# Optimization experiments

Hardware: AMD Instinct MI355X
Metric: run time of the kernel (lower is better)

## Reference

```python
import jax, jax.numpy as jnp
import numpy as np

T = 2048
HID = 5120
NH = 16
D_NOPE = 128
D_ROPE = 64
D_V = 128
Q_LORA = 1536
KV_LORA = 512
THETA = 10000.0
EPS = 1e-6
QK_HD = D_NOPE + D_ROPE
SCALE = QK_HD ** -0.5


def setup_inputs() -> dict:
    key = jax.random.key(0)
    ks = jax.random.split(key, 8)
    s = 0.02  # weight init scale for numerical stability
    return {
        "positions": jnp.arange(T, dtype=jnp.int32),
        "hidden_states": jax.random.normal(ks[0], (T, HID), jnp.float32),
        "w_qa": jax.random.normal(ks[1], (HID, Q_LORA), jnp.float32) * s,
        "qa_ln_w": jnp.ones((Q_LORA,), jnp.float32),
        "w_qb": jax.random.normal(ks[2], (Q_LORA, NH * QK_HD), jnp.float32) * s,
        "w_kva": jax.random.normal(ks[3], (HID, KV_LORA + D_ROPE), jnp.float32) * s,
        "kva_ln_w": jnp.ones((KV_LORA,), jnp.float32),
        "w_kvb": jax.random.normal(ks[4], (KV_LORA, NH * (D_NOPE + D_V)), jnp.float32) * s,
        "w_o": jax.random.normal(ks[5], (NH * D_V, HID), jnp.float32) * s,
    }


def rmsnorm(x, w):
    var = jnp.mean(x * x, axis=-1, keepdims=True)
    return x * jax.lax.rsqrt(var + EPS) * w


def apply_rope(positions, x):
    # GPT-J (interleaved) style rope on last dim of size D_ROPE; x: [T, H, D_ROPE]
    inv_freq = 1.0 / (THETA ** (jnp.arange(0, D_ROPE, 2, dtype=jnp.float32) / D_ROPE))
    ang = positions.astype(jnp.float32)[:, None] * inv_freq  # [T, D_ROPE/2]
    cos = jnp.cos(ang)[:, None, :]  # [T, 1, D/2]
    sin = jnp.sin(ang)[:, None, :]
    x1 = x[..., 0::2]
    x2 = x[..., 1::2]
    o1 = x1 * cos - x2 * sin
    o2 = x2 * cos + x1 * sin
    return jnp.stack([o1, o2], axis=-1).reshape(x.shape)


def reference(positions, hidden_states, w_qa, qa_ln_w, w_qb, w_kva, kva_ln_w, w_kvb, w_o):
    # --- low-rank Q path ---
    q_c = rmsnorm(hidden_states @ w_qa, qa_ln_w)             # [T, Q_LORA]
    q = (q_c @ w_qb).reshape(T, NH, QK_HD)                   # [T, H, 192]
    q_nope, q_pe = q[..., :D_NOPE], q[..., D_NOPE:]

    # --- compressed KV path ---
    kv = hidden_states @ w_kva                               # [T, KV_LORA + D_ROPE]
    kv_c = rmsnorm(kv[:, :KV_LORA], kva_ln_w)                # [T, 512]
    k_pe = kv[:, KV_LORA:][:, None, :]                       # [T, 1, 64]

    # partial rope
    q_pe = apply_rope(positions, q_pe)                       # [T, H, 64]
    k_pe = apply_rope(positions, k_pe)                       # [T, 1, 64]

    # decompress K_nope / V
    kv_up = (kv_c @ w_kvb).reshape(T, NH, D_NOPE + D_V)
    k_nope, v = kv_up[..., :D_NOPE], kv_up[..., D_NOPE:]     # [T, H, 128] each

    k_pe_b = jnp.broadcast_to(k_pe, (T, NH, D_ROPE))
    q_full = jnp.concatenate([q_nope, q_pe], axis=-1)        # [T, H, 192]
    k_full = jnp.concatenate([k_nope, k_pe_b], axis=-1)      # [T, H, 192]

    # causal attention
    scores = jnp.einsum("thd,shd->hts", q_full, k_full) * SCALE  # [H, T, T]
    causal = positions[:, None] >= positions[None, :]
    scores = jnp.where(causal[None], scores, jnp.finfo(scores.dtype).min)
    probs = jax.nn.softmax(scores, axis=-1)
    attn = jnp.einsum("hts,shd->thd", probs, v)              # [T, H, 128]

    out = attn.reshape(T, NH * D_V) @ w_o                    # [T, HID]
    return out
```

## Files before the change

kernel.cpp:

```cpp
#include <hip/hip_runtime.h>
#include <hip/hip_bf16.h>
#include <math.h>

#define T 2048
#define HID 5120
#define NH 16
#define D_NOPE 128
#define D_ROPE 64
#define D_V 128
#define Q_LORA 1536
#define KV_LORA 512
#define QK_HD 192
#define KVA_N 576
#define KVA_NP 640
#define N_QB (NH*QK_HD)
#define N_KVB (NH*(D_NOPE+D_V))
#define ATT_SCALE 0.07216878364870322f

typedef __bf16 bf16x8_t __attribute__((ext_vector_type(8)));
typedef float f32x4_t __attribute__((ext_vector_type(4)));
typedef unsigned short u16x4 __attribute__((ext_vector_type(4)));
typedef unsigned int u32x4 __attribute__((ext_vector_type(4)));

union BF8 { u16x4 h[2]; unsigned short u[8]; bf16x8_t v; u32x4 q; };

static __device__ __forceinline__ unsigned short f2bf(float f){
  union { float f; unsigned u; } x; x.f = f;
  unsigned r = x.u + 0x7FFFu + ((x.u >> 16) & 1u);
  return (unsigned short)(r >> 16);
}

static __device__ __forceinline__ void gload_lds16(const void* g, void* l){
  __builtin_amdgcn_global_load_lds(
      (const __attribute__((address_space(1))) void*)(unsigned long long)g,
      (__attribute__((address_space(3))) void*)(unsigned int)(unsigned long long)l,
      16, 0, 0);
}

__global__ __launch_bounds__(256) void k_cvt(const float* __restrict__ in,
                                             unsigned short* __restrict__ out, int n4){
  int i = blockIdx.x*256 + threadIdx.x;
  int stride = gridDim.x*256;
  for (; i < n4; i += stride){
    f32x4_t v = ((const f32x4_t*)in)[i];
    u16x4 o; o.x=f2bf(v.x); o.y=f2bf(v.y); o.z=f2bf(v.z); o.w=f2bf(v.w);
    ((u16x4*)out)[i] = o;
  }
}

__global__ __launch_bounds__(256) void k_cvtT(const float* __restrict__ W,
                                              unsigned short* __restrict__ Wt, int K, int N){
  __shared__ float tile[32][33];
  int n0 = blockIdx.x*32, k0 = blockIdx.y*32;
  int r = threadIdx.x >> 3, c4 = (threadIdx.x & 7) * 4;
  f32x4_t v = {0.f,0.f,0.f,0.f};
  if (n0 + c4 < N) v = *(const f32x4_t*)(W + (size_t)(k0 + r)*N + n0 + c4);
  tile[r][c4+0]=v.x; tile[r][c4+1]=v.y; tile[r][c4+2]=v.z; tile[r][c4+3]=v.w;
  __syncthreads();
  u16x4 o;
  o.x = f2bf(tile[c4+0][r]); o.y = f2bf(tile[c4+1][r]);
  o.z = f2bf(tile[c4+2][r]); o.w = f2bf(tile[c4+3][r]);
  *(u16x4*)(Wt + (size_t)(n0 + r)*K + k0 + c4) = o;
}

__global__ __launch_bounds__(256) void k_gemm(const unsigned short* __restrict__ A,
                                              const unsigned short* __restrict__ Bt,
                                              float* __restrict__ C, int M, int N, int K){
  __shared__ unsigned short sA[128*32];
  __shared__ unsigned short sB[128*32];
  int bn = blockIdx.x*128, bm = blockIdx.y*128;
  int tid = threadIdx.x;
  int l = tid & 63, lr = l & 15, lg = l >> 4;
  int w = tid >> 6;
  int wm = (w >> 1)*64, wn = (w & 1)*64;
  f32x4_t acc[4][4];
  f32x4_t z4 = {0.f,0.f,0.f,0.f};
  #pragma unroll
  for (int i=0;i<4;i++)
    #pragma unroll
    for(int j=0;j<4;j++) acc[i][j] = z4;
  for (int k0 = 0; k0 < K; k0 += 32){
    __syncthreads();
    #pragma unroll
    for (int it = 0; it < 2; ++it){
      int c = it*256 + tid;
      int row = c >> 2, kc = (c & 3) * 8;
      gload_lds16(A  + (size_t)(bm + row)*K + k0 + kc, &sA[c*8]);
      gload_lds16(Bt + (size_t)(bn + row)*K + k0 + kc, &sB[c*8]);
    }
    __syncthreads();
    BF8 af[4], bf[4];
    #pragma unroll
    for (int mf=0; mf<4; ++mf)
      af[mf].q = *(const u32x4*)&sA[(wm + mf*16 + lr)*32 + 8*lg];
    #pragma unroll
    for (int nf=0; nf<4; ++nf)
      bf[nf].q = *(const u32x4*)&sB[(wn + nf*16 + lr)*32 + 8*lg];
    #pragma unroll
    for (int mf=0; mf<4; ++mf)
      #pragma unroll
      for (int nf=0; nf<4; ++nf)
        acc[mf][nf] = __builtin_amdgcn_mfma_f32_16x16x32_bf16(af[mf].v, bf[nf].v, acc[mf][nf], 0,0,0);
  }
  #pragma unroll
  for (int mf=0; mf<4; ++mf){
    int row = bm + wm + mf*16 + 4*lg;
    #pragma unroll
    for (int nf=0; nf<4; ++nf){
      int col = bn + wn + nf*16 + lr;
      #pragma unroll
      for (int rg=0; rg<4; ++rg)
        C[(size_t)(row + rg)*N + col] = acc[mf][nf][rg];
    }
  }
}

__global__ __launch_bounds__(256) void k_rms_q(const float* __restrict__ qa,
                                               const float* __restrict__ w,
                                               unsigned short* __restrict__ qc){
  int t = blockIdx.x, tid = threadIdx.x;
  const float* row = qa + (size_t)t*Q_LORA;
  float ss = 0.f;
  for (int i = tid; i < Q_LORA; i += 256){ float x = row[i]; ss += x*x; }
  #pragma unroll
  for (int off=1; off<64; off<<=1) ss += __shfl_xor(ss, off, 64);
  __shared__ float red[4];
  if ((tid & 63) == 0) red[tid>>6] = ss;
  __syncthreads();
  ss = red[0]+red[1]+red[2]+red[3];
  float sc = rsqrtf(ss/(float)Q_LORA + 1e-6f);
  unsigned short* orow = qc + (size_t)t*Q_LORA;
  for (int i = tid; i < Q_LORA; i += 256) orow[i] = f2bf(row[i]*sc*w[i]);
}

__global__ __launch_bounds__(256) void k_rms_kv(const float* __restrict__ kvf,
                                                const float* __restrict__ w,
                                                const int* __restrict__ pos,
                                                unsigned short* __restrict__ kvc,
                                                unsigned short* __restrict__ k_full){
  int t = blockIdx.x, tid = threadIdx.x;
  const float* row = kvf + (size_t)t*KVA_NP;
  float ss = 0.f;
  for (int i = tid; i < KV_LORA; i += 256){ float x = row[i]; ss += x*x; }
  #pragma unroll
  for (int off=1; off<64; off<<=1) ss += __shfl_xor(ss, off, 64);
  __shared__ float red[4];
  if ((tid & 63) == 0) red[tid>>6] = ss;
  __syncthreads();
  ss = red[0]+red[1]+red[2]+red[3];
  float sc = rsqrtf(ss/(float)KV_LORA + 1e-6f);
  for (int i = tid; i < KV_LORA; i += 256)
    kvc[(size_t)t*KV_LORA + i] = f2bf(row[i]*sc*w[i]);
  if (tid < 32){
    int i = tid;
    float x1 = row[KV_LORA + 2*i], x2 = row[KV_LORA + 2*i + 1];
    float p = (float)pos[t];
    float invf = 1.0f / powf(10000.0f, (float)(2*i)/64.0f);
    float sn, cs; sincosf(p*invf, &sn, &cs);
    unsigned short b1 = f2bf(x1*cs - x2*sn), b2 = f2bf(x2*cs + x1*sn);
    for (int h=0; h<NH; ++h){
      unsigned short* kr = k_full + ((size_t)(h*T + t))*QK_HD + D_NOPE + 2*i;
      kr[0] = b1; kr[1] = b2;
    }
  }
}

__global__ __launch_bounds__(256) void k_scat_q(const float* __restrict__ qf,
                                                const int* __restrict__ pos,
                                                unsigned short* __restrict__ q_full){
  int t = blockIdx.x, tid = threadIdx.x;
  const float* row = qf + (size_t)t*N_QB;
  for (int idx = tid; idx < NH*D_NOPE; idx += 256){
    int h = idx >> 7, d = idx & 127;
    q_full[((size_t)(h*T + t))*QK_HD + d] = f2bf(row[h*QK_HD + d] * ATT_SCALE);
  }
  float p = (float)pos[t];
  for (int idx = tid; idx < NH*32; idx += 256){
    int h = idx >> 5, i = idx & 31;
    float x1 = row[h*QK_HD + D_NOPE + 2*i], x2 = row[h*QK_HD + D_NOPE + 2*i+1];
    float invf = 1.0f / powf(10000.0f, (float)(2*i)/64.0f);
    float sn, cs; sincosf(p*invf, &sn, &cs);
    unsigned short* qr = q_full + ((size_t)(h*T + t))*QK_HD + D_NOPE + 2*i;
    qr[0] = f2bf((x1*cs - x2*sn)*ATT_SCALE);
    qr[1] = f2bf((x2*cs + x1*sn)*ATT_SCALE);
  }
}

__global__ __launch_bounds__(256) void k_scat_kv(const float* __restrict__ kvup,
                                                 unsigned short* __restrict__ k_full,
                                                 unsigned short* __restrict__ vt){
  int h = blockIdx.y, t0 = blockIdx.x*32;
  int tid = threadIdx.x;
  __shared__ float vtile[32][129];
  #pragma unroll
  for (int it=0; it<16; ++it){
    int idx = tid + it*256;
    int r = idx >> 7, d = idx & 127;
    float kn = kvup[(size_t)(t0 + r)*N_KVB + h*256 + d];
    k_full[((size_t)(h*T + t0 + r))*QK_HD + d] = f2bf(kn);
    vtile[r][d] = kvup[(size_t)(t0 + r)*N_KVB + h*256 + 128 + d];
  }
  __syncthreads();
  int d = tid >> 1, half = tid & 1;
  unsigned short* vrow = vt + ((size_t)(h*128 + d))*T + t0 + half*16;
  #pragma unroll
  for (int c=0; c<4; ++c){
    u16x4 o;
    o.x = f2bf(vtile[half*16 + c*4 + 0][d]);
    o.y = f2bf(vtile[half*16 + c*4 + 1][d]);
    o.z = f2bf(vtile[half*16 + c*4 + 2][d]);
    o.w = f2bf(vtile[half*16 + c*4 + 3][d]);
    *(u16x4*)(vrow + c*4) = o;
  }
}

__global__ __launch_bounds__(256,1) void k_attn(const unsigned short* __restrict__ q_full,
                                                const unsigned short* __restrict__ k_full,
                                                const unsigned short* __restrict__ vt,
                                                unsigned short* __restrict__ attn){
  __shared__ unsigned short K_lds[2][3*64*8*8];
  __shared__ unsigned short P_t[4][16][68];
  int bid = blockIdx.x;
  int h  = ((bid & 7) << 1) | ((bid >> 3) & 1);
  int qp = bid >> 4;
  int qtA = qp, qtB = 31 - qp;
  int ntiles = qtB + 1;
  int tid = threadIdx.x, w = tid >> 6, l = tid & 63, lr = l & 15, lg = l >> 4;
  int qrowA = qtA*64 + w*16 + lr;
  int qrowB = qtB*64 + w*16 + lr;
  BF8 qfA[6], qfB[6];
  {
    const unsigned short* qa = q_full + ((size_t)(h*T + qrowA))*QK_HD + 8*lg;
    const unsigned short* qb = q_full + ((size_t)(h*T + qrowB))*QK_HD + 8*lg;
    #pragma unroll
    for (int dk=0; dk<6; ++dk){
      qfA[dk].q = *(const u32x4*)(qa + dk*32);
      qfB[dk].q = *(const u32x4*)(qb + dk*32);
    }
  }
  float mA = -1e30f, lA = 0.f, mB = -1e30f, lB = 0.f;
  f32x4_t z4 = {0.f,0.f,0.f,0.f};
  f32x4_t oA[8], oB[8];
  #pragma unroll
  for (int i=0;i<8;i++){ oA[i] = z4; oB[i] = z4; }

  const unsigned short* kbase = k_full + (size_t)h*T*QK_HD;
  auto stageK = [&](int b, int t){
    #pragma unroll
    for (int is=0; is<6; ++is){
      int c = is*256 + tid;
      int chunk3 = c >> 9, row = (c >> 3) & 63, slot = c & 7;
      gload_lds16(kbase + (size_t)(t*64 + row)*QK_HD + chunk3*64 + ((slot ^ (row & 7))*8),
                  &K_lds[b][c*8]);
    }
  };
  stageK(0, 0);
  __syncthreads();
  int p = 0;
  int pslot0 = lg ^ (lr & 7), pslot1 = (4 + lg) ^ (lr & 7);
  for (int t = 0; t < ntiles; ++t){
    int s0 = t*64;
    BF8 va[8][2];
    #pragma unroll
    for (int df=0; df<8; ++df){
      const unsigned short* vp = vt + ((size_t)(h*D_V + df*16 + lr))*T + s0 + 8*lg;
      va[df][0].q = *(const u32x4*)(vp);
      va[df][1].q = *(const u32x4*)(vp + 32);
    }
    if (t+1 < ntiles) stageK(p^1, t+1);
    bool actA = (t <= qtA);
    f32x4_t sA[4], sB[4];
    #pragma unroll
    for (int i=0;i<4;i++){ sA[i] = z4; sB[i] = z4; }
    #pragma unroll
    for (int sfi=0; sfi<4; ++sfi){
      int rbase = (sfi*16 + lr)*8;
      #pragma unroll
      for (int dk=0; dk<6; ++dk){
        int ps = (dk & 1) ? pslot1 : pslot0;
        BF8 a; a.q = *(const u32x4*)&K_lds[p][(((dk>>1)*64*8) + rbase + ps)*8];
        sB[sfi] = __builtin_amdgcn_mfma_f32_16x16x32_bf16(a.v, qfB[dk].v, sB[sfi], 0,0,0);
        if (actA)
          sA[sfi] = __builtin_amdgcn_mfma_f32_16x16x32_bf16(a.v, qfA[dk].v, sA[sfi], 0,0,0);
      }
    }
    {
      bool diag = (t == ntiles-1);
      float tmax = -1e30f;
      #pragma unroll
      for (int sfi=0; sfi<4; ++sfi){
        #pragma unroll
        for (int rg=0; rg<4; ++rg){
          int s_g = s0 + sfi*16 + 4*lg + rg;
          float v = sB[sfi][rg];
          if (diag && s_g > qrowB) v = -1e30f;
          sB[sfi][rg] = v;
          tmax = fmaxf(tmax, v);
        }
      }
      tmax = fmaxf(tmax, __shfl_xor(tmax, 16, 64));
      tmax = fmaxf(tmax, __shfl_xor(tmax, 32, 64));
      float m_new = fmaxf(mB, tmax);
      float alpha = __expf(mB - m_new);
      float psum = 0.f;
      #pragma unroll
      for (int sfi=0; sfi<4; ++sfi){
        #pragma unroll
        for (int rg=0; rg<4; ++rg){
          float pv = __expf(sB[sfi][rg] - m_new);
          psum += pv;
          P_t[w][lr][sfi*16 + 4*lg + rg] = f2bf(pv);
        }
      }
      psum += __shfl_xor(psum, 16, 64);
      psum += __shfl_xor(psum, 32, 64);
      lB = lB*alpha + psum;
      mB = m_new;
      BF8 bp[2];
      #pragma unroll
      for (int ks=0; ks<2; ++ks){
        bp[ks].h[0] = *(const u16x4*)&P_t[w][lr][ks*32 + 8*lg];
        bp[ks].h[1] = *(const u16x4*)&P_t[w][lr][ks*32 + 8*lg + 4];
      }
      #pragma unroll
      for (int df=0; df<8; ++df){
        oB[df][0]*=alpha; oB[df][1]*=alpha; oB[df][2]*=alpha; oB[df][3]*=alpha;
        oB[df] = __builtin_amdgcn_mfma_f32_16x16x32_bf16(va[df][0].v, bp[0].v, oB[df], 0,0,0);
        oB[df] = __builtin_amdgcn_mfma_f32_16x16x32_bf16(va[df][1].v, bp[1].v, oB[df], 0,0,0);
      }
    }
    if (actA){
      bool diag = (t == qtA);
      float tmax = -1e30f;
      #pragma unroll
      for (int sfi=0; sfi<4; ++sfi){
        #pragma unroll
        for (int rg=0; rg<4; ++rg){
          int s_g = s0 + sfi*16 + 4*lg + rg;
          float v = sA[sfi][rg];
          if (diag && s_g > qrowA) v = -1e30f;
          sA[sfi][rg] = v;
          tmax = fmaxf(tmax, v);
        }
      }
      tmax = fmaxf(tmax, __shfl_xor(tmax, 16, 64));
      tmax = fmaxf(tmax, __shfl_xor(tmax, 32, 64));
      float m_new = fmaxf(mA, tmax);
      float alpha = __expf(mA - m_new);
      float psum = 0.f;
      #pragma unroll
      for (int sfi=0; sfi<4; ++sfi){
        #pragma unroll
        for (int rg=0; rg<4; ++rg){
          float pv = __expf(sA[sfi][rg] - m_new);
          psum += pv;
          P_t[w][lr][sfi*16 + 4*lg + rg] = f2bf(pv);
        }
      }
      psum += __shfl_xor(psum, 16, 64);
      psum += __shfl_xor(psum, 32, 64);
      lA = lA*alpha + psum;
      mA = m_new;
      BF8 bp[2];
      #pragma unroll
      for (int ks=0; ks<2; ++ks){
        bp[ks].h[0] = *(const u16x4*)&P_t[w][lr][ks*32 + 8*lg];
        bp[ks].h[1] = *(const u16x4*)&P_t[w][lr][ks*32 + 8*lg + 4];
      }
      #pragma unroll
      for (int df=0; df<8; ++df){
        oA[df][0]*=alpha; oA[df][1]*=alpha; oA[df][2]*=alpha; oA[df][3]*=alpha;
        oA[df] = __builtin_amdgcn_mfma_f32_16x16x32_bf16(va[df][0].v, bp[0].v, oA[df], 0,0,0);
        oA[df] = __builtin_amdgcn_mfma_f32_16x16x32_bf16(va[df][1].v, bp[1].v, oA[df], 0,0,0);
      }
    }
    __syncthreads();
    p ^= 1;
  }
  float invA = 1.0f / lA, invB = 1.0f / lB;
  #pragma unroll
  for (int df=0; df<8; ++df){
    u16x4 ov;
    ov.x = f2bf(oA[df][0]*invA); ov.y = f2bf(oA[df][1]*invA);
    ov.z = f2bf(oA[df][2]*invA); ov.w = f2bf(oA[df][3]*invA);
    *(u16x4*)(attn + (size_t)qrowA*(NH*D_V) + h*D_V + df*16 + 4*lg) = ov;
    ov.x = f2bf(oB[df][0]*invB); ov.y = f2bf(oB[df][1]*invB);
    ov.z = f2bf(oB[df][2]*invB); ov.w = f2bf(oB[df][3]*invB);
    *(u16x4*)(attn + (size_t)qrowB*(NH*D_V) + h*D_V + df*16 + 4*lg) = ov;
  }
}

extern "C" void kernel_launch(void* const* d_in, const int* in_sizes, int n_in,
                              void* d_out, int out_size, void* d_ws, size_t ws_size,
                              hipStream_t stream){
  const int*   positions = (const int*)d_in[0];
  const float* hidden = (const float*)d_in[1];
  const float* w_qa   = (const float*)d_in[2];
  const float* qa_ln  = (const float*)d_in[3];
  const float* w_qb   = (const float*)d_in[4];
  const float* w_kva  = (const float*)d_in[5];
  const float* kva_ln = (const float*)d_in[6];
  const float* w_kvb  = (const float*)d_in[7];
  const float* w_o    = (const float*)d_in[8];
  float* out = (float*)d_out;

  char* p = (char*)d_ws;
  auto alloc = [&](size_t bytes){ void* r = (void*)p; p += (bytes + 255) & ~(size_t)255; return r; };
  unsigned short* hb     = (unsigned short*)alloc((size_t)T*HID*2);
  unsigned short* wqaT   = (unsigned short*)alloc((size_t)Q_LORA*HID*2);
  unsigned short* wqbT   = (unsigned short*)alloc((size_t)N_QB*Q_LORA*2);
  unsigned short* wkvaT  = (unsigned short*)alloc((size_t)KVA_NP*HID*2);
  unsigned short* wkvbT  = (unsigned short*)alloc((size_t)N_KVB*KV_LORA*2);
  unsigned short* woT    = (unsigned short*)alloc((size_t)HID*(NH*D_V)*2);
  float* q_a             = (float*)alloc((size_t)T*Q_LORA*4);
  unsigned short* q_c    = (unsigned short*)alloc((size_t)T*Q_LORA*2);
  float* qf              = (float*)alloc((size_t)T*N_QB*4);
  float* kvf             = (float*)alloc((size_t)T*KVA_NP*4);
  unsigned short* kv_c   = (unsigned short*)alloc((size_t)T*KV_LORA*2);
  float* kvupf           = (float*)alloc((size_t)T*N_KVB*4);
  unsigned short* q_full = (unsigned short*)alloc((size_t)NH*T*QK_HD*2);
  unsigned short* k_full = (unsigned short*)alloc((size_t)NH*T*QK_HD*2);
  unsigned short* vt     = (unsigned short*)alloc((size_t)NH*D_V*T*2);
  unsigned short* attnb  = (unsigned short*)alloc((size_t)T*NH*D_V*2);

  k_cvt<<<2048, 256, 0, stream>>>(hidden, hb, T*HID/4);
  k_cvtT<<<dim3(Q_LORA/32, HID/32), 256, 0, stream>>>(w_qa, wqaT, HID, Q_LORA);
  k_cvtT<<<dim3(N_QB/32, Q_LORA/32), 256, 0, stream>>>(w_qb, wqbT, Q_LORA, N_QB);
  k_cvtT<<<dim3(KVA_NP/32, HID/32), 256, 0, stream>>>(w_kva, wkvaT, HID, KVA_N);
  k_cvtT<<<dim3(N_KVB/32, KV_LORA/32), 256, 0, stream>>>(w_kvb, wkvbT, KV_LORA, N_KVB);
  k_cvtT<<<dim3(HID/32, (NH*D_V)/32), 256, 0, stream>>>(w_o, woT, NH*D_V, HID);

  k_gemm<<<dim3(Q_LORA/128, T/128), 256, 0, stream>>>(hb, wqaT, q_a, T, Q_LORA, HID);
  k_rms_q<<<T, 256, 0, stream>>>(q_a, qa_ln, q_c);
  k_gemm<<<dim3(N_QB/128, T/128), 256, 0, stream>>>(q_c, wqbT, qf, T, N_QB, Q_LORA);
  k_gemm<<<dim3(KVA_NP/128, T/128), 256, 0, stream>>>(hb, wkvaT, kvf, T, KVA_NP, HID);
  k_rms_kv<<<T, 256, 0, stream>>>(kvf, kva_ln, positions, kv_c, k_full);
  k_gemm<<<dim3(N_KVB/128, T/128), 256, 0, stream>>>(kv_c, wkvbT, kvupf, T, N_KVB, KV_LORA);
  k_scat_q<<<T, 256, 0, stream>>>(qf, positions, q_full);
  k_scat_kv<<<dim3(T/32, NH), 256, 0, stream>>>(kvupf, k_full, vt);
  k_attn<<<256, 256, 0, stream>>>(q_full, k_full, vt, attnb);
  k_gemm<<<dim3(HID/128, T/128), 256, 0, stream>>>(attnb, woT, out, T, HID, NH*D_V);
}
```

Baseline: 715.3 us.

## Fuse Q/KV down-projection GEMMs, add split-K with reductions, swizzle GEMM tiles

Merges the w_qa and w_kva projections into one GEMM over a concatenated transposed weight so the hidden states are streamed once. Adds split-K (3-way for the fused down-projection, 2-way for the q up-projection), writing partial sums to a buffer that new reduction kernels combine; the q reduction is fused with RoPE and scaling, replacing the old scatter kernel. Adds an XCD-style workgroup swizzle so neighbouring tiles land on the same chiplet for cache reuse. The trade-off is extra fp32 partial-sum traffic and extra reduction launches in exchange for more workgroups in flight on the smaller GEMMs.

```diff
diff --git a/kernel.cpp b/kernel.cpp
--- a/kernel.cpp
+++ b/kernel.cpp
@@ -13,6 +13,7 @@
 #define QK_HD 192
 #define KVA_N 576
 #define KVA_NP 640
+#define N_QKVA (Q_LORA + KVA_NP)
 #define N_QB (NH*QK_HD)
 #define N_KVB (NH*(D_NOPE+D_V))
 #define ATT_SCALE 0.07216878364870322f
@@ -65,10 +66,19 @@
 
 __global__ __launch_bounds__(256) void k_gemm(const unsigned short* __restrict__ A,
                                               const unsigned short* __restrict__ Bt,
-                                              float* __restrict__ C, int M, int N, int K){
+                                              float* __restrict__ C,
+                                              int M, int N, int K, int kChunk){
   __shared__ unsigned short sA[128*32];
   __shared__ unsigned short sB[128*32];
-  int bn = blockIdx.x*128, bm = blockIdx.y*128;
+  int gx = gridDim.x;
+  int nwg = gx*gridDim.y;
+  int id = blockIdx.x + gx*blockIdx.y;
+  int cpx = nwg >> 3;
+  int swz = (id & 7)*cpx + (id >> 3);
+  int bn = (swz % gx)*128, bm = (swz / gx)*128;
+  int kBeg = blockIdx.z*kChunk;
+  int kEnd = kBeg + kChunk; if (kEnd > K) kEnd = K;
+  float* Cs = C + (size_t)blockIdx.z*M*N;
   int tid = threadIdx.x;
   int l = tid & 63, lr = l & 15, lg = l >> 4;
   int w = tid >> 6;
@@ -79,7 +89,7 @@
   for (int i=0;i<4;i++)
     #pragma unroll
     for(int j=0;j<4;j++) acc[i][j] = z4;
-  for (int k0 = 0; k0 < K; k0 += 32){
+  for (int k0 = kBeg; k0 < kEnd; k0 += 32){
     __syncthreads();
     #pragma unroll
     for (int it = 0; it < 2; ++it){
@@ -110,16 +120,52 @@
       int col = bn + wn + nf*16 + lr;
       #pragma unroll
       for (int rg=0; rg<4; ++rg)
-        C[(size_t)(row + rg)*N + col] = acc[mf][nf][rg];
-    }
-  }
-}
-
-__global__ __launch_bounds__(256) void k_rms_q(const float* __restrict__ qa,
+        Cs[(size_t)(row + rg)*N + col] = acc[mf][nf][rg];
+    }
+  }
+}
+
+__global__ __launch_bounds__(256) void k_red3(const float* __restrict__ P,
+                                              float* __restrict__ out, int n4){
+  const size_t sstr = (size_t)T*N_QKVA/4;
+  int i = blockIdx.x*256 + threadIdx.x, stride = gridDim.x*256;
+  const f32x4_t* p4 = (const f32x4_t*)P;
+  f32x4_t* o4 = (f32x4_t*)out;
+  for (; i < n4; i += stride)
+    o4[i] = p4[i] + p4[i+sstr] + p4[i+2*sstr];
+}
+
+__global__ __launch_bounds__(256) void k_red_q(const float* __restrict__ P,
+                                               const int* __restrict__ pos,
+                                               unsigned short* __restrict__ q_full){
+  int t = blockIdx.x, tid = threadIdx.x;
+  const float* r0 = P + (size_t)t*N_QB;
+  const float* r1 = r0 + (size_t)T*N_QB;
+  float p = (float)pos[t];
+  for (int idx = tid; idx < NH*160; idx += 256){
+    int h = idx/160, j = idx - h*160;
+    if (j < 128){
+      float v = (r0[h*QK_HD + j] + r1[h*QK_HD + j]) * ATT_SCALE;
+      q_full[((size_t)(h*T + t))*QK_HD + j] = f2bf(v);
+    } else {
+      int i = j - 128;
+      int d0 = D_NOPE + 2*i;
+      float x1 = r0[h*QK_HD + d0]   + r1[h*QK_HD + d0];
+      float x2 = r0[h*QK_HD + d0+1] + r1[h*QK_HD + d0+1];
+      float invf = 1.0f / powf(10000.0f, (float)(2*i)/64.0f);
+      float sn, cs; sincosf(p*invf, &sn, &cs);
+      unsigned short* qr = q_full + ((size_t)(h*T + t))*QK_HD + d0;
+      qr[0] = f2bf((x1*cs - x2*sn)*ATT_SCALE);
+      qr[1] = f2bf((x2*cs + x1*sn)*ATT_SCALE);
+    }
+  }
+}
+
+__global__ __launch_bounds__(256) void k_rms_q(const float* __restrict__ qkva,
                                                const float* __restrict__ w,
                                                unsigned short* __restrict__ qc){
   int t = blockIdx.x, tid = threadIdx.x;
-  const float* row = qa + (size_t)t*Q_LORA;
+  const float* row = qkva + (size_t)t*N_QKVA;
   float ss = 0.f;
   for (int i = tid; i < Q_LORA; i += 256){ float x = row[i]; ss += x*x; }
   #pragma unroll
@@ -133,13 +179,13 @@
   for (int i = tid; i < Q_LORA; i += 256) orow[i] = f2bf(row[i]*sc*w[i]);
 }
 
-__global__ __launch_bounds__(256) void k_rms_kv(const float* __restrict__ kvf,
+__global__ __launch_bounds__(256) void k_rms_kv(const float* __restrict__ qkva,
                                                 const float* __restrict__ w,
                                                 const int* __restrict__ pos,
                                                 unsigned short* __restrict__ kvc,
                                                 unsigned short* __restrict__ k_full){
   int t = blockIdx.x, tid = threadIdx.x;
-  const float* row = kvf + (size_t)t*KVA_NP;
+  const float* row = qkva + (size_t)t*N_QKVA + Q_LORA;
   float ss = 0.f;
   for (int i = tid; i < KV_LORA; i += 256){ float x = row[i]; ss += x*x; }
   #pragma unroll
@@ -165,27 +211,6 @@
   }
 }
 
-__global__ __launch_bounds__(256) void k_scat_q(const float* __restrict__ qf,
-                                                const int* __restrict__ pos,
-                                                unsigned short* __restrict__ q_full){
-  int t = blockIdx.x, tid = threadIdx.x;
-  const float* row = qf + (size_t)t*N_QB;
-  for (int idx = tid; idx < NH*D_NOPE; idx += 256){
-    int h = idx >> 7, d = idx & 127;
-    q_full[((size_t)(h*T + t))*QK_HD + d] = f2bf(row[h*QK_HD + d] * ATT_SCALE);
-  }
-  float p = (float)pos[t];
-  for (int idx = tid; idx < NH*32; idx += 256){
-    int h = idx >> 5, i = idx & 31;
-    float x1 = row[h*QK_HD + D_NOPE + 2*i], x2 = row[h*QK_HD + D_NOPE + 2*i+1];
-    float invf = 1.0f / powf(10000.0f, (float)(2*i)/64.0f);
-    float sn, cs; sincosf(p*invf, &sn, &cs);
-    unsigned short* qr = q_full + ((size_t)(h*T + t))*QK_HD + D_NOPE + 2*i;
-    qr[0] = f2bf((x1*cs - x2*sn)*ATT_SCALE);
-    qr[1] = f2bf((x2*cs + x1*sn)*ATT_SCALE);
-  }
-}
-
 __global__ __launch_bounds__(256) void k_scat_kv(const float* __restrict__ kvup,
                                                  unsigned short* __restrict__ k_full,
                                                  unsigned short* __restrict__ vt){
@@ -406,38 +431,36 @@
 
   char* p = (char*)d_ws;
   auto alloc = [&](size_t bytes){ void* r = (void*)p; p += (bytes + 255) & ~(size_t)255; return r; };
-  unsigned short* hb     = (unsigned short*)alloc((size_t)T*HID*2);
-  unsigned short* wqaT   = (unsigned short*)alloc((size_t)Q_LORA*HID*2);
-  unsigned short* wqbT   = (unsigned short*)alloc((size_t)N_QB*Q_LORA*2);
-  unsigned short* wkvaT  = (unsigned short*)alloc((size_t)KVA_NP*HID*2);
-  unsigned short* wkvbT  = (unsigned short*)alloc((size_t)N_KVB*KV_LORA*2);
-  unsigned short* woT    = (unsigned short*)alloc((size_t)HID*(NH*D_V)*2);
-  float* q_a             = (float*)alloc((size_t)T*Q_LORA*4);
-  unsigned short* q_c    = (unsigned short*)alloc((size_t)T*Q_LORA*2);
-  float* qf              = (float*)alloc((size_t)T*N_QB*4);
-  float* kvf             = (float*)alloc((size_t)T*KVA_NP*4);
-  unsigned short* kv_c   = (unsigned short*)alloc((size_t)T*KV_LORA*2);
-  float* kvupf           = (float*)alloc((size_t)T*N_KVB*4);
-  unsigned short* q_full = (unsigned short*)alloc((size_t)NH*T*QK_HD*2);
-  unsigned short* k_full = (unsigned short*)alloc((size_t)NH*T*QK_HD*2);
-  unsigned short* vt     = (unsigned short*)alloc((size_t)NH*D_V*T*2);
-  unsigned short* attnb  = (unsigned short*)alloc((size_t)T*NH*D_V*2);
+  unsigned short* hb      = (unsigned short*)alloc((size_t)T*HID*2);
+  unsigned short* wqkvaT  = (unsigned short*)alloc((size_t)N_QKVA*HID*2);
+  unsigned short* wqbT    = (unsigned short*)alloc((size_t)N_QB*Q_LORA*2);
+  unsigned short* wkvbT   = (unsigned short*)alloc((size_t)N_KVB*KV_LORA*2);
+  unsigned short* woT     = (unsigned short*)alloc((size_t)HID*(NH*D_V)*2);
+  float* qkva             = (float*)alloc((size_t)T*N_QKVA*4);
+  unsigned short* q_c     = (unsigned short*)alloc((size_t)T*Q_LORA*2);
+  unsigned short* kv_c    = (unsigned short*)alloc((size_t)T*KV_LORA*2);
+  unsigned short* q_full  = (unsigned short*)alloc((size_t)NH*T*QK_HD*2);
+  unsigned short* k_full  = (unsigned short*)alloc((size_t)NH*T*QK_HD*2);
+  unsigned short* vt      = (unsigned short*)alloc((size_t)NH*D_V*T*2);
+  unsigned short* attnb   = (unsigned short*)alloc((size_t)T*NH*D_V*2);
+  float* Pbuf             = (float*)alloc((size_t)3*T*N_QKVA*4);
+  float* kvupf            = Pbuf;
 
   k_cvt<<<2048, 256, 0, stream>>>(hidden, hb, T*HID/4);
-  k_cvtT<<<dim3(Q_LORA/32, HID/32), 256, 0, stream>>>(w_qa, wqaT, HID, Q_LORA);
+  k_cvtT<<<dim3(Q_LORA/32, HID/32), 256, 0, stream>>>(w_qa, wqkvaT, HID, Q_LORA);
+  k_cvtT<<<dim3(KVA_NP/32, HID/32), 256, 0, stream>>>(w_kva, wqkvaT + (size_t)Q_LORA*HID, HID, KVA_N);
   k_cvtT<<<dim3(N_QB/32, Q_LORA/32), 256, 0, stream>>>(w_qb, wqbT, Q_LORA, N_QB);
-  k_cvtT<<<dim3(KVA_NP/32, HID/32), 256, 0, stream>>>(w_kva, wkvaT, HID, KVA_N);
   k_cvtT<<<dim3(N_KVB/32, KV_LORA/32), 256, 0, stream>>>(w_kvb, wkvbT, KV_LORA, N_KVB);
   k_cvtT<<<dim3(HID/32, (NH*D_V)/32), 256, 0, stream>>>(w_o, woT, NH*D_V, HID);
 
-  k_gemm<<<dim3(Q_LORA/128, T/128), 256, 0, stream>>>(hb, wqaT, q_a, T, Q_LORA, HID);
-  k_rms_q<<<T, 256, 0, stream>>>(q_a, qa_ln, q_c);
-  k_gemm<<<dim3(N_QB/128, T/128), 256, 0, stream>>>(q_c, wqbT, qf, T, N_QB, Q_LORA);
-  k_gemm<<<dim3(KVA_NP/128, T/128), 256, 0, stream>>>(hb, wkvaT, kvf, T, KVA_NP, HID);
-  k_rms_kv<<<T, 256, 0, stream>>>(kvf, kva_ln, positions, kv_c, k_full);
-  k_gemm<<<dim3(N_KVB/128, T/128), 256, 0, stream>>>(kv_c, wkvbT, kvupf, T, N_KVB, KV_LORA);
-  k_scat_q<<<T, 256, 0, stream>>>(qf, positions, q_full);
+  k_gemm<<<dim3(N_QKVA/128, T/128, 3), 256, 0, stream>>>(hb, wqkvaT, Pbuf, T, N_QKVA, HID, 1728);
+  k_red3<<<1024, 256, 0, stream>>>(Pbuf, qkva, T*N_QKVA/4);
+  k_rms_q<<<T, 256, 0, stream>>>(qkva, qa_ln, q_c);
+  k_rms_kv<<<T, 256, 0, stream>>>(qkva, kva_ln, positions, kv_c, k_full);
+  k_gemm<<<dim3(N_QB/128, T/128, 2), 256, 0, stream>>>(q_c, wqbT, Pbuf, T, N_QB, Q_LORA, 768);
+  k_red_q<<<T, 256, 0, stream>>>(Pbuf, positions, q_full);
+  k_gemm<<<dim3(N_KVB/128, T/128, 1), 256, 0, stream>>>(kv_c, wkvbT, kvupf, T, N_KVB, KV_LORA, KV_LORA);
   k_scat_kv<<<dim3(T/32, NH), 256, 0, stream>>>(kvupf, k_full, vt);
   k_attn<<<256, 256, 0, stream>>>(q_full, k_full, vt, attnb);
-  k_gemm<<<dim3(HID/128, T/128), 256, 0, stream>>>(attnb, woT, out, T, HID, NH*D_V);
-}
+  k_gemm<<<dim3(HID/128, T/128, 1), 256, 0, stream>>>(attnb, woT, out, T, HID, NH*D_V, NH*D_V);
+}
```

Result: faster. 582.5 us (-18.6%).
